# Performance work log

Measured on AMD Instinct MI355X. Metric: run time of the kernel, lower is better.

## Reference

```python
import jax, jax.numpy as jnp
import numpy as np

# Dimensions (from init_kwargs)
B, Q, C = 2, 40000, 128      # batch, BEV queries (200x200), d_model
NH, NP = 8, 4                 # n_heads, n_points per head
H, W = 90, 160                # value feature-map spatial shape (len = H*W)
HD = C // NH                  # head dim


def setup_inputs() -> dict:
    key = jax.random.key(0)
    ks = jax.random.split(key, 8)
    s = 0.02
    return {
        "query": jax.random.normal(ks[0], (B, Q, C), jnp.float32),
        "value": jax.random.normal(ks[1], (B, H * W, C), jnp.float32),
        "ref_points": jax.random.uniform(ks[2], (B, Q, 2), jnp.float32),  # normalized [0,1] (x, y)
        "W_value": jax.random.normal(ks[3], (C, C), jnp.float32) * s,
        "b_value": jnp.zeros((C,), jnp.float32),
        "W_offset": jax.random.normal(ks[4], (C, NH * NP * 2), jnp.float32) * s,
        "b_offset": jnp.zeros((NH * NP * 2,), jnp.float32),
        "W_attn": jax.random.normal(ks[5], (C, NH * NP), jnp.float32) * s,
        "b_attn": jnp.zeros((NH * NP,), jnp.float32),
        "W_out": jax.random.normal(ks[6], (C, C), jnp.float32) * s,
        "b_out": jnp.zeros((C,), jnp.float32),
    }


def _bilinear_sample(value, loc):
    """value: [B, H*W, NH, HD]; loc: [B, Q, NH, NP, 2] normalized in [0,1].
    Bilinear grid-sample with zero padding outside (align_corners=False).
    Returns [B, Q, NH, NP, HD]."""
    x = loc[..., 0] * W - 0.5
    y = loc[..., 1] * H - 0.5
    x0 = jnp.floor(x)
    y0 = jnp.floor(y)
    wx = x - x0
    wy = y - y0
    x0i = x0.astype(jnp.int32)
    y0i = y0.astype(jnp.int32)
    v = jnp.transpose(value, (0, 2, 1, 3))  # [B, NH, HW, HD] for per-head gather

    def corner(xi, yi, w):
        valid = ((xi >= 0) & (xi < W) & (yi >= 0) & (yi < H)).astype(value.dtype)
        idx = jnp.clip(yi, 0, H - 1) * W + jnp.clip(xi, 0, W - 1)  # [B, Q, NH, NP]
        i = jnp.transpose(idx, (0, 2, 1, 3))                        # [B, NH, Q, NP]
        g = jax.vmap(jax.vmap(lambda vb, ib: vb[ib]))(v, i)         # [B, NH, Q, NP, HD]
        g = jnp.transpose(g, (0, 2, 1, 3, 4))                       # [B, Q, NH, NP, HD]
        return g * (w * valid)[..., None]

    return (corner(x0i, y0i, (1.0 - wx) * (1.0 - wy))
            + corner(x0i + 1, y0i, wx * (1.0 - wy))
            + corner(x0i, y0i + 1, (1.0 - wx) * wy)
            + corner(x0i + 1, y0i + 1, wx * wy))


def reference(query, value, ref_points, W_value, b_value, W_offset, b_offset,
              W_attn, b_attn, W_out, b_out):
    # value projection, split into heads
    v = (value @ W_value + b_value).reshape(B, H * W, NH, HD)
    # per-query learned sampling offsets (in pixels) and attention weights
    offsets = (query @ W_offset + b_offset).reshape(B, Q, NH, NP, 2)
    attn = jax.nn.softmax((query @ W_attn + b_attn).reshape(B, Q, NH, NP), axis=-1)
    # sampling locations, normalized
    norm = jnp.array([W, H], jnp.float32)
    loc = ref_points[:, :, None, None, :] + offsets / norm  # [B, Q, NH, NP, 2]
    sampled = _bilinear_sample(v, loc)                       # [B, Q, NH, NP, HD]
    agg = jnp.einsum('bqhpd,bqhp->bqhd', sampled, attn).reshape(B, Q, C)
    return agg @ W_out + b_out
```

## Files before the change

### kernel.cpp

```cpp
#include <hip/hip_runtime.h>
#include <hip/hip_bf16.h>

#define BB 2
#define QQ 40000
#define CC 128
#define NHH 8
#define NPP 4
#define HH 90
#define WW 160
#define HWW (HH*WW)
#define BQ (BB*QQ)
#define BHW (BB*HWW)

typedef __attribute__((ext_vector_type(8))) short short8;
typedef __attribute__((ext_vector_type(4))) float f32x4;

static __device__ inline short f2bf(float f) {
    __hip_bfloat16 h = __float2bfloat16(f);
    return __builtin_bit_cast(short, h);
}

__global__ __launch_bounds__(256) void prep_weights(
    const float* __restrict__ Wv, const float* __restrict__ Wo,
    const float* __restrict__ Wa, const float* __restrict__ Wout,
    const float* __restrict__ bo, const float* __restrict__ ba,
    short* __restrict__ wtv, short* __restrict__ wcat,
    short* __restrict__ woutt, float* __restrict__ bcat)
{
    const int t = blockIdx.x * 256 + threadIdx.x;
    const int stride = gridDim.x * 256;
    for (int i = t; i < 128 * 128; i += stride) {
        int n = i >> 7, k = i & 127;
        wtv[i] = f2bf(Wv[k * 128 + n]);
    }
    for (int i = t; i < 96 * 128; i += stride) {
        int n = i >> 7, k = i & 127;
        float w = (n < 64) ? Wo[k * 64 + n] : Wa[k * 32 + (n - 64)];
        wcat[i] = f2bf(w);
    }
    for (int i = t; i < 128 * 128; i += stride) {
        int n = i >> 7, k = i & 127;
        woutt[i] = f2bf(Wout[k * 128 + n]);
    }
    if (t < 96) bcat[t] = (t < 64) ? bo[t] : ba[t - 64];
}

template<int N, bool XF32, bool OUT_BF16>
__global__ __launch_bounds__(256, 2) void gemm_pipe(
    const void* __restrict__ Xv, const short* __restrict__ Wt,
    const float* __restrict__ bias, void* __restrict__ Yv, int ntiles)
{
    constexpr int CT = N / 32;
    __shared__ short sW[N * 128];
    __shared__ short sX[128 * 128];
    const int tid = threadIdx.x;

    for (int i = tid; i < N * 16; i += 256) {
        int nn = i >> 4, c8 = (i & 15) * 8;
        short8 wv = reinterpret_cast<const short8*>(Wt)[i];
        *(short8*)((char*)sW + ((nn * 256 + c8 * 2) ^ ((nn & 7) << 4))) = wv;
    }

    const int lane = tid & 63, wid = tid >> 6;
    const int wr = wid >> 1, wc = wid & 1;
    const int l15 = lane & 15, lg = lane >> 4;

    float bvc[CT];
    #pragma unroll
    for (int ct = 0; ct < CT; ++ct) bvc[ct] = bias[wc * (N / 2) + ct * 16 + l15];

    float4 xf[16];
    short8 xb[8];

    int tile = blockIdx.x;
    if (tile < ntiles) {
        if (XF32) {
            const float4* src = reinterpret_cast<const float4*>((const float*)Xv) + (long)tile * 4096;
            #pragma unroll
            for (int j = 0; j < 16; ++j) xf[j] = src[j * 256 + tid];
        } else {
            const short8* src = reinterpret_cast<const short8*>((const short*)Xv) + (long)tile * 2048;
            #pragma unroll
            for (int j = 0; j < 8; ++j) xb[j] = src[j * 256 + tid];
        }
    }

    for (; tile < ntiles; tile += gridDim.x) {
        __syncthreads();
        if (XF32) {
            #pragma unroll
            for (int j = 0; j < 16; ++j) {
                int flat = j * 256 + tid;
                int row = flat >> 5, c4 = flat & 31;
                int byo = (row * 256 + c4 * 8) ^ ((row & 7) << 4);
                short* p = (short*)((char*)sX + byo);
                p[0] = f2bf(xf[j].x); p[1] = f2bf(xf[j].y);
                p[2] = f2bf(xf[j].z); p[3] = f2bf(xf[j].w);
            }
        } else {
            #pragma unroll
            for (int j = 0; j < 8; ++j) {
                int flat = j * 256 + tid;
                int row = flat >> 4, c8 = flat & 15;
                int byo = (row * 256 + c8 * 16) ^ ((row & 7) << 4);
                *(short8*)((char*)sX + byo) = xb[j];
            }
        }
        int nt = tile + gridDim.x;
        if (nt < ntiles) {
            if (XF32) {
                const float4* src = reinterpret_cast<const float4*>((const float*)Xv) + (long)nt * 4096;
                #pragma unroll
                for (int j = 0; j < 16; ++j) xf[j] = src[j * 256 + tid];
            } else {
                const short8* src = reinterpret_cast<const short8*>((const short*)Xv) + (long)nt * 2048;
                #pragma unroll
                for (int j = 0; j < 8; ++j) xb[j] = src[j * 256 + tid];
            }
        }
        __syncthreads();

        f32x4 acc[4][CT] = {};
        #pragma unroll
        for (int ks = 0; ks < 4; ++ks) {
            short8 a[4], b[CT];
            #pragma unroll
            for (int rt = 0; rt < 4; ++rt) {
                int row = wr * 64 + rt * 16 + l15;
                a[rt] = *(const short8*)((const char*)sX +
                        ((row * 256 + ks * 64 + lg * 16) ^ ((row & 7) << 4)));
            }
            #pragma unroll
            for (int ct = 0; ct < CT; ++ct) {
                int n = wc * (N / 2) + ct * 16 + l15;
                b[ct] = *(const short8*)((const char*)sW +
                        ((n * 256 + ks * 64 + lg * 16) ^ ((n & 7) << 4)));
            }
            #pragma unroll
            for (int rt = 0; rt < 4; ++rt)
                #pragma unroll
                for (int ct = 0; ct < CT; ++ct)
                    acc[rt][ct] = __builtin_amdgcn_mfma_f32_16x16x32_bf16(
                        a[rt], b[ct], acc[rt][ct], 0, 0, 0);
        }

        const long r0 = (long)tile * 128;
        #pragma unroll
        for (int rt = 0; rt < 4; ++rt) {
            #pragma unroll
            for (int ct = 0; ct < CT; ++ct) {
                int col = wc * (N / 2) + ct * 16 + l15;
                #pragma unroll
                for (int r = 0; r < 4; ++r) {
                    long row = r0 + wr * 64 + rt * 16 + lg * 4 + r;
                    float val = acc[rt][ct][r] + bvc[ct];
                    if (OUT_BF16) ((short*)Yv)[row * N + col] = f2bf(val);
                    else          ((float*)Yv)[row * N + col] = val;
                }
            }
        }
    }
}

__global__ __launch_bounds__(256) void deform_sample(
    const short* __restrict__ v,
    const float* __restrict__ qp,
    const float* __restrict__ ref,
    unsigned* __restrict__ agg)
{
    const int bq   = blockIdx.x * 4 + (threadIdx.x >> 6);
    const int lane = threadIdx.x & 63;
    const int h  = lane >> 3;
    const int dp = lane & 7;
    const int bsel = (bq >= QQ) ? 1 : 0;

    const float rx = ref[(long)bq * 2 + 0] * (float)WW - 0.5f;
    const float ry = ref[(long)bq * 2 + 1] * (float)HH - 0.5f;

    const float* al = qp + (long)bq * 96 + 64 + h * 4;
    float l0 = al[0], l1 = al[1], l2 = al[2], l3 = al[3];
    float m = fmaxf(fmaxf(l0, l1), fmaxf(l2, l3));
    float e0 = __expf(l0 - m), e1 = __expf(l1 - m);
    float e2 = __expf(l2 - m), e3 = __expf(l3 - m);
    float inv = 1.0f / (e0 + e1 + e2 + e3);
    float aw[4] = { e0 * inv, e1 * inv, e2 * inv, e3 * inv };

    const float* ob = qp + (long)bq * 96 + h * 8;
    const short* vb = v + (long)bsel * HWW * 128 + h * 16 + dp * 2;

    float acc0 = 0.0f, acc1 = 0.0f;
    #pragma unroll
    for (int p = 0; p < NPP; ++p) {
        float x = rx + ob[p * 2 + 0];
        float y = ry + ob[p * 2 + 1];
        float x0f = floorf(x), y0f = floorf(y);
        float wx = x - x0f, wy = y - y0f;
        int ix0 = (int)x0f, iy0 = (int)y0f;
        float a = aw[p];
        #pragma unroll
        for (int cy = 0; cy < 2; ++cy) {
            int iy = iy0 + cy;
            float wyc = cy ? wy : (1.0f - wy);
            bool vy = ((unsigned)iy < (unsigned)HH);
            int iyc = min(max(iy, 0), HH - 1);
            #pragma unroll
            for (int cx = 0; cx < 2; ++cx) {
                int ix = ix0 + cx;
                float wxc = cx ? wx : (1.0f - wx);
                bool vx = ((unsigned)ix < (unsigned)WW);
                int ixc = min(max(ix, 0), WW - 1);
                float wgt = (vx && vy) ? (a * wxc * wyc) : 0.0f;
                unsigned u = *reinterpret_cast<const unsigned*>(
                    vb + ((long)iyc * WW + ixc) * 128);
                float g0 = __builtin_bit_cast(float, u << 16);
                float g1 = __builtin_bit_cast(float, u & 0xffff0000u);
                acc0 += wgt * g0;
                acc1 += wgt * g1;
            }
        }
    }
    unsigned pk = (unsigned)(unsigned short)f2bf(acc0)
                | ((unsigned)(unsigned short)f2bf(acc1) << 16);
    agg[(long)bq * 64 + lane] = pk;
}

extern "C" void kernel_launch(void* const* d_in, const int* in_sizes, int n_in,
                              void* d_out, int out_size, void* d_ws, size_t ws_size,
                              hipStream_t stream) {
    const float* query = (const float*)d_in[0];
    const float* value = (const float*)d_in[1];
    const float* ref   = (const float*)d_in[2];
    const float* Wv    = (const float*)d_in[3];
    const float* bv    = (const float*)d_in[4];
    const float* Wo    = (const float*)d_in[5];
    const float* bo    = (const float*)d_in[6];
    const float* Wa    = (const float*)d_in[7];
    const float* ba    = (const float*)d_in[8];
    const float* Wout  = (const float*)d_in[9];
    const float* bout  = (const float*)d_in[10];
    float* out = (float*)d_out;

    char* ws = (char*)d_ws;
    short* vbf   = (short*)ws;  ws += (long)BHW * 128 * 2;
    short* wtv   = (short*)ws;  ws += 128 * 128 * 2;
    short* wcat  = (short*)ws;  ws += 96 * 128 * 2;
    short* woutt = (short*)ws;  ws += 128 * 128 * 2;
    float* bcat  = (float*)ws;  ws += 128 * 4;
    float* qp    = (float*)ws;  ws += (long)BQ * 96 * 4;
    unsigned* aggb = (unsigned*)ws;

    const int ntV = BHW / 128;
    const int ntQ = BQ / 128;
    const int gV = ntV < 512 ? ntV : 512;
    const int gQ = ntQ < 512 ? ntQ : 512;

    prep_weights<<<64, 256, 0, stream>>>(Wv, Wo, Wa, Wout, bo, ba,
                                         wtv, wcat, woutt, bcat);
    gemm_pipe<128, true, true><<<gV, 256, 0, stream>>>(value, wtv, bv, vbf, ntV);
    gemm_pipe<96, true, false><<<gQ, 256, 0, stream>>>(query, wcat, bcat, qp, ntQ);
    deform_sample<<<BQ / 4, 256, 0, stream>>>(vbf, qp, ref, aggb);
    gemm_pipe<128, false, false><<<gQ, 256, 0, stream>>>(aggb, woutt, bout, out, ntQ);
}
```

Before: 170.5 us.

## Fuse deformable sampling with output projection and store query projections as bf16

The sampling kernel and the output projection GEMM become one kernel. Each block samples 128 queries into a swizzled shared-memory bf16 tile, then multiplies it by the shared-memory output weights with MFMA, so the aggregated tensor no longer makes a round trip through global memory. Each lane now gathers 8 bf16 channels per corner with one 16-byte load instead of 2 channels, and the offset and logit projection is written in bf16 rather than fp32. The costs are lower precision for the offsets and logits, 64KB of LDS per block that limits occupancy, and fewer threads in flight to hide gather latency.

After: 164.1 us. 3.8% less time.

```diff
diff --git a/kernel.cpp b/kernel.cpp
--- a/kernel.cpp
+++ b/kernel.cpp
@@ -13,11 +13,15 @@
 #define BHW (BB*HWW)
 
 typedef __attribute__((ext_vector_type(8))) short short8;
+typedef __attribute__((ext_vector_type(4))) unsigned short ushortx4;
 typedef __attribute__((ext_vector_type(4))) float f32x4;
 
 static __device__ inline short f2bf(float f) {
     __hip_bfloat16 h = __float2bfloat16(f);
     return __builtin_bit_cast(short, h);
+}
+static __device__ inline float bfu(unsigned short u) {
+    return __builtin_bit_cast(float, ((unsigned)u) << 16);
 }
 
 __global__ __launch_bounds__(256) void prep_weights(
@@ -162,66 +166,128 @@
     }
 }
 
-__global__ __launch_bounds__(256) void deform_sample(
+__global__ __launch_bounds__(256, 2) void sample_out(
     const short* __restrict__ v,
-    const float* __restrict__ qp,
+    const short* __restrict__ qp,
     const float* __restrict__ ref,
-    unsigned* __restrict__ agg)
+    const short* __restrict__ Wt,
+    const float* __restrict__ bias,
+    float* __restrict__ out)
 {
-    const int bq   = blockIdx.x * 4 + (threadIdx.x >> 6);
-    const int lane = threadIdx.x & 63;
-    const int h  = lane >> 3;
-    const int dp = lane & 7;
-    const int bsel = (bq >= QQ) ? 1 : 0;
-
-    const float rx = ref[(long)bq * 2 + 0] * (float)WW - 0.5f;
-    const float ry = ref[(long)bq * 2 + 1] * (float)HH - 0.5f;
-
-    const float* al = qp + (long)bq * 96 + 64 + h * 4;
-    float l0 = al[0], l1 = al[1], l2 = al[2], l3 = al[3];
-    float m = fmaxf(fmaxf(l0, l1), fmaxf(l2, l3));
-    float e0 = __expf(l0 - m), e1 = __expf(l1 - m);
-    float e2 = __expf(l2 - m), e3 = __expf(l3 - m);
-    float inv = 1.0f / (e0 + e1 + e2 + e3);
-    float aw[4] = { e0 * inv, e1 * inv, e2 * inv, e3 * inv };
-
-    const float* ob = qp + (long)bq * 96 + h * 8;
-    const short* vb = v + (long)bsel * HWW * 128 + h * 16 + dp * 2;
-
-    float acc0 = 0.0f, acc1 = 0.0f;
+    __shared__ short sAgg[128 * 128];
+    __shared__ short sW[128 * 128];
+    const int tid = threadIdx.x;
+    const int lane = tid & 63, wid = tid >> 6;
+    const long tile0 = (long)blockIdx.x * 128;
+
+    for (int i = tid; i < 128 * 16; i += 256) {
+        int nn = i >> 4, c8 = (i & 15) * 8;
+        short8 wv = reinterpret_cast<const short8*>(Wt)[i];
+        *(short8*)((char*)sW + ((nn * 256 + c8 * 2) ^ ((nn & 7) << 4))) = wv;
+    }
+
+    const int q4 = lane >> 4;
+    const int l  = lane & 15;
+    const int h  = l >> 1;
+
     #pragma unroll
-    for (int p = 0; p < NPP; ++p) {
-        float x = rx + ob[p * 2 + 0];
-        float y = ry + ob[p * 2 + 1];
-        float x0f = floorf(x), y0f = floorf(y);
-        float wx = x - x0f, wy = y - y0f;
-        int ix0 = (int)x0f, iy0 = (int)y0f;
-        float a = aw[p];
-        #pragma unroll
-        for (int cy = 0; cy < 2; ++cy) {
-            int iy = iy0 + cy;
-            float wyc = cy ? wy : (1.0f - wy);
-            bool vy = ((unsigned)iy < (unsigned)HH);
-            int iyc = min(max(iy, 0), HH - 1);
-            #pragma unroll
-            for (int cx = 0; cx < 2; ++cx) {
-                int ix = ix0 + cx;
-                float wxc = cx ? wx : (1.0f - wx);
-                bool vx = ((unsigned)ix < (unsigned)WW);
-                int ixc = min(max(ix, 0), WW - 1);
-                float wgt = (vx && vy) ? (a * wxc * wyc) : 0.0f;
-                unsigned u = *reinterpret_cast<const unsigned*>(
-                    vb + ((long)iyc * WW + ixc) * 128);
-                float g0 = __builtin_bit_cast(float, u << 16);
-                float g1 = __builtin_bit_cast(float, u & 0xffff0000u);
-                acc0 += wgt * g0;
-                acc1 += wgt * g1;
-            }
-        }
-    }
-    unsigned pk = (unsigned)(unsigned short)f2bf(acc0)
-                | ((unsigned)(unsigned short)f2bf(acc1) << 16);
-    agg[(long)bq * 64 + lane] = pk;
+    for (int pass = 0; pass < 8; ++pass) {
+        const int lq = wid * 32 + pass * 4 + q4;
+        const long bq = tile0 + lq;
+        const int bsel = (bq >= QQ) ? 1 : 0;
+
+        const float rx = ref[bq * 2 + 0] * (float)WW - 0.5f;
+        const float ry = ref[bq * 2 + 1] * (float)HH - 0.5f;
+
+        const short* qpb = qp + bq * 96;
+        ushortx4 lg4 = *reinterpret_cast<const ushortx4*>(qpb + 64 + h * 4);
+        float l0 = bfu(lg4[0]), l1 = bfu(lg4[1]), l2 = bfu(lg4[2]), l3 = bfu(lg4[3]);
+        float m = fmaxf(fmaxf(l0, l1), fmaxf(l2, l3));
+        float e0 = __expf(l0 - m), e1 = __expf(l1 - m);
+        float e2 = __expf(l2 - m), e3 = __expf(l3 - m);
+        float inv = 1.0f / (e0 + e1 + e2 + e3);
+        float aw[4] = { e0 * inv, e1 * inv, e2 * inv, e3 * inv };
+
+        short8 ob = *reinterpret_cast<const short8*>(qpb + h * 8);
+        float ofs[8];
+        #pragma unroll
+        for (int j = 0; j < 8; ++j) ofs[j] = bfu((unsigned short)ob[j]);
+
+        const short* vb = v + (long)bsel * HWW * 128 + l * 8;
+
+        float ac[8] = {0,0,0,0,0,0,0,0};
+        #pragma unroll
+        for (int p = 0; p < NPP; ++p) {
+            float x = rx + ofs[p * 2 + 0];
+            float y = ry + ofs[p * 2 + 1];
+            float x0f = floorf(x), y0f = floorf(y);
+            float wx = x - x0f, wy = y - y0f;
+            int ix0 = (int)x0f, iy0 = (int)y0f;
+            float wxs[2] = { 1.0f - wx, wx };
+            float wys[2] = { 1.0f - wy, wy };
+            #pragma unroll
+            for (int cy = 0; cy < 2; ++cy) {
+                int iy = iy0 + cy;
+                bool vy = ((unsigned)iy < (unsigned)HH);
+                int iyc = min(max(iy, 0), HH - 1);
+                #pragma unroll
+                for (int cx = 0; cx < 2; ++cx) {
+                    int ix = ix0 + cx;
+                    bool vx = ((unsigned)ix < (unsigned)WW);
+                    int ixc = min(max(ix, 0), WW - 1);
+                    float wgt = (vx && vy) ? (aw[p] * wxs[cx] * wys[cy]) : 0.0f;
+                    short8 g = *reinterpret_cast<const short8*>(vb + (iyc * WW + ixc) * 128);
+                    #pragma unroll
+                    for (int j = 0; j < 8; ++j)
+                        ac[j] += wgt * bfu((unsigned short)g[j]);
+                }
+            }
+        }
+        short8 pk;
+        #pragma unroll
+        for (int j = 0; j < 8; ++j) pk[j] = f2bf(ac[j]);
+        *(short8*)((char*)sAgg + ((lq * 256 + l * 16) ^ ((lq & 7) << 4))) = pk;
+    }
+    __syncthreads();
+
+    const int wr = wid >> 1, wc = wid & 1;
+    const int l15 = lane & 15, lg = lane >> 4;
+    f32x4 acc[4][4] = {};
+    #pragma unroll
+    for (int ks = 0; ks < 4; ++ks) {
+        short8 a[4], b[4];
+        #pragma unroll
+        for (int rt = 0; rt < 4; ++rt) {
+            int row = wr * 64 + rt * 16 + l15;
+            a[rt] = *(const short8*)((const char*)sAgg +
+                    ((row * 256 + ks * 64 + lg * 16) ^ ((row & 7) << 4)));
+        }
+        #pragma unroll
+        for (int ct = 0; ct < 4; ++ct) {
+            int n = wc * 64 + ct * 16 + l15;
+            b[ct] = *(const short8*)((const char*)sW +
+                    ((n * 256 + ks * 64 + lg * 16) ^ ((n & 7) << 4)));
+        }
+        #pragma unroll
+        for (int rt = 0; rt < 4; ++rt)
+            #pragma unroll
+            for (int ct = 0; ct < 4; ++ct)
+                acc[rt][ct] = __builtin_amdgcn_mfma_f32_16x16x32_bf16(
+                    a[rt], b[ct], acc[rt][ct], 0, 0, 0);
+    }
+    #pragma unroll
+    for (int rt = 0; rt < 4; ++rt) {
+        #pragma unroll
+        for (int ct = 0; ct < 4; ++ct) {
+            int col = wc * 64 + ct * 16 + l15;
+            float bv = bias[col];
+            #pragma unroll
+            for (int r = 0; r < 4; ++r) {
+                long row = tile0 + wr * 64 + rt * 16 + lg * 4 + r;
+                out[row * 128 + col] = acc[rt][ct][r] + bv;
+            }
+        }
+    }
 }
 
 extern "C" void kernel_launch(void* const* d_in, const int* in_sizes, int n_in,
@@ -246,8 +312,7 @@
     short* wcat  = (short*)ws;  ws += 96 * 128 * 2;
     short* woutt = (short*)ws;  ws += 128 * 128 * 2;
     float* bcat  = (float*)ws;  ws += 128 * 4;
-    float* qp    = (float*)ws;  ws += (long)BQ * 96 * 4;
-    unsigned* aggb = (unsigned*)ws;
+    short* qpb   = (short*)ws;
 
     const int ntV = BHW / 128;
     const int ntQ = BQ / 128;
@@ -257,7 +322,6 @@
     prep_weights<<<64, 256, 0, stream>>>(Wv, Wo, Wa, Wout, bo, ba,
                                          wtv, wcat, woutt, bcat);
     gemm_pipe<128, true, true><<<gV, 256, 0, stream>>>(value, wtv, bv, vbf, ntV);
-    gemm_pipe<96, true, false><<<gQ, 256, 0, stream>>>(query, wcat, bcat, qp, ntQ);
-    deform_sample<<<BQ / 4, 256, 0, stream>>>(vbf, qp, ref, aggb);
-    gemm_pipe<128, false, false><<<gQ, 256, 0, stream>>>(aggb, woutt, bout, out, ntQ);
-}
+    gemm_pipe<96, true, true><<<gQ, 256, 0, stream>>>(query, wcat, bcat, qpb, ntQ);
+    sample_out<<<ntQ, 256, 0, stream>>>(vbf, qpb, ref, woutt, bout, out);
+}
```

## Store query projections in bf16 and sample 8 channels per thread

Applied to the files above, without the earlier changes.

The offset/attention projection now writes bf16 instead of fp32, which halves that intermediate buffer and its reads. The sampling kernel is remapped from one 64-lane wavefront per query with 2 channels per lane to 16 threads per query with 8 channels per lane, using 16-byte vector loads of value corners and a 16-byte store of the aggregate. Each thread now does more gathers and arithmetic, and more queries share a wavefront. Offsets in bf16 lose precision (pixel offsets rounded to about 8 mantissa bits), which may shift sampling locations slightly.

After: 161.6 us. -5.2%, faster.

```diff
diff --git a/kernel.cpp b/kernel.cpp
--- a/kernel.cpp
+++ b/kernel.cpp
@@ -13,11 +13,15 @@
 #define BHW (BB*HWW)
 
 typedef __attribute__((ext_vector_type(8))) short short8;
+typedef __attribute__((ext_vector_type(4))) unsigned short ushortx4;
 typedef __attribute__((ext_vector_type(4))) float f32x4;
 
 static __device__ inline short f2bf(float f) {
     __hip_bfloat16 h = __float2bfloat16(f);
     return __builtin_bit_cast(short, h);
+}
+static __device__ inline float bfu(unsigned short u) {
+    return __builtin_bit_cast(float, ((unsigned)u) << 16);
 }
 
 __global__ __launch_bounds__(256) void prep_weights(
@@ -162,66 +166,69 @@
     }
 }
 
-__global__ __launch_bounds__(256) void deform_sample(
+__global__ __launch_bounds__(256) void deform_sample16(
     const short* __restrict__ v,
-    const float* __restrict__ qp,
+    const short* __restrict__ qp,
     const float* __restrict__ ref,
-    unsigned* __restrict__ agg)
+    short* __restrict__ agg)
 {
-    const int bq   = blockIdx.x * 4 + (threadIdx.x >> 6);
-    const int lane = threadIdx.x & 63;
-    const int h  = lane >> 3;
-    const int dp = lane & 7;
-    const int bsel = (bq >= QQ) ? 1 : 0;
-
-    const float rx = ref[(long)bq * 2 + 0] * (float)WW - 0.5f;
-    const float ry = ref[(long)bq * 2 + 1] * (float)HH - 0.5f;
-
-    const float* al = qp + (long)bq * 96 + 64 + h * 4;
-    float l0 = al[0], l1 = al[1], l2 = al[2], l3 = al[3];
+    const int t = blockIdx.x * 256 + threadIdx.x;
+    const long q = t >> 4;
+    const int l = t & 15;
+    const int h = l >> 1;
+    const int bsel = (q >= QQ) ? 1 : 0;
+
+    const float rx = ref[q * 2 + 0] * (float)WW - 0.5f;
+    const float ry = ref[q * 2 + 1] * (float)HH - 0.5f;
+
+    const short* qpb = qp + q * 96;
+    ushortx4 lg4 = *reinterpret_cast<const ushortx4*>(qpb + 64 + h * 4);
+    float l0 = bfu(lg4[0]), l1 = bfu(lg4[1]), l2 = bfu(lg4[2]), l3 = bfu(lg4[3]);
     float m = fmaxf(fmaxf(l0, l1), fmaxf(l2, l3));
     float e0 = __expf(l0 - m), e1 = __expf(l1 - m);
     float e2 = __expf(l2 - m), e3 = __expf(l3 - m);
     float inv = 1.0f / (e0 + e1 + e2 + e3);
     float aw[4] = { e0 * inv, e1 * inv, e2 * inv, e3 * inv };
 
-    const float* ob = qp + (long)bq * 96 + h * 8;
-    const short* vb = v + (long)bsel * HWW * 128 + h * 16 + dp * 2;
-
-    float acc0 = 0.0f, acc1 = 0.0f;
+    short8 ob = *reinterpret_cast<const short8*>(qpb + h * 8);
+    float ofs[8];
+    #pragma unroll
+    for (int j = 0; j < 8; ++j) ofs[j] = bfu((unsigned short)ob[j]);
+
+    const short* vb = v + (long)bsel * HWW * 128 + l * 8;
+
+    float ac[8] = {0,0,0,0,0,0,0,0};
     #pragma unroll
     for (int p = 0; p < NPP; ++p) {
-        float x = rx + ob[p * 2 + 0];
-        float y = ry + ob[p * 2 + 1];
+        float x = rx + ofs[p * 2 + 0];
+        float y = ry + ofs[p * 2 + 1];
         float x0f = floorf(x), y0f = floorf(y);
         float wx = x - x0f, wy = y - y0f;
         int ix0 = (int)x0f, iy0 = (int)y0f;
-        float a = aw[p];
+        float wxs[2] = { 1.0f - wx, wx };
+        float wys[2] = { 1.0f - wy, wy };
         #pragma unroll
         for (int cy = 0; cy < 2; ++cy) {
             int iy = iy0 + cy;
-            float wyc = cy ? wy : (1.0f - wy);
             bool vy = ((unsigned)iy < (unsigned)HH);
             int iyc = min(max(iy, 0), HH - 1);
             #pragma unroll
             for (int cx = 0; cx < 2; ++cx) {
                 int ix = ix0 + cx;
-                float wxc = cx ? wx : (1.0f - wx);
                 bool vx = ((unsigned)ix < (unsigned)WW);
                 int ixc = min(max(ix, 0), WW - 1);
-                float wgt = (vx && vy) ? (a * wxc * wyc) : 0.0f;
-                unsigned u = *reinterpret_cast<const unsigned*>(
-                    vb + ((long)iyc * WW + ixc) * 128);
-                float g0 = __builtin_bit_cast(float, u << 16);
-                float g1 = __builtin_bit_cast(float, u & 0xffff0000u);
-                acc0 += wgt * g0;
-                acc1 += wgt * g1;
-            }
-        }
-    }
-    unsigned pk = (unsigned)(unsigned short)f2bf(acc0)
-                | ((unsigned)(unsigned short)f2bf(acc1) << 16);
-    agg[(long)bq * 64 + lane] = pk;
+                float wgt = (vx && vy) ? (aw[p] * wxs[cx] * wys[cy]) : 0.0f;
+                short8 g = *reinterpret_cast<const short8*>(vb + (iyc * WW + ixc) * 128);
+                #pragma unroll
+                for (int j = 0; j < 8; ++j)
+                    ac[j] += wgt * bfu((unsigned short)g[j]);
+            }
+        }
+    }
+    short8 pk;
+    #pragma unroll
+    for (int j = 0; j < 8; ++j) pk[j] = f2bf(ac[j]);
+    *reinterpret_cast<short8*>(agg + q * 128 + l * 8) = pk;
 }
 
 extern "C" void kernel_launch(void* const* d_in, const int* in_sizes, int n_in,
@@ -246,8 +253,8 @@
     short* wcat  = (short*)ws;  ws += 96 * 128 * 2;
     short* woutt = (short*)ws;  ws += 128 * 128 * 2;
     float* bcat  = (float*)ws;  ws += 128 * 4;
-    float* qp    = (float*)ws;  ws += (long)BQ * 96 * 4;
-    unsigned* aggb = (unsigned*)ws;
+    short* qpb   = (short*)ws;  ws += (long)BQ * 96 * 2;
+    short* aggb  = (short*)ws;
 
     const int ntV = BHW / 128;
     const int ntQ = BQ / 128;
@@ -257,7 +264,7 @@
     prep_weights<<<64, 256, 0, stream>>>(Wv, Wo, Wa, Wout, bo, ba,
                                          wtv, wcat, woutt, bcat);
     gemm_pipe<128, true, true><<<gV, 256, 0, stream>>>(value, wtv, bv, vbf, ntV);
-    gemm_pipe<96, true, false><<<gQ, 256, 0, stream>>>(query, wcat, bcat, qp, ntQ);
-    deform_sample<<<BQ / 4, 256, 0, stream>>>(vbf, qp, ref, aggb);
+    gemm_pipe<96, true, true><<<gQ, 256, 0, stream>>>(query, wcat, bcat, qpb, ntQ);
+    deform_sample16<<<(BQ * 16) / 256, 256, 0, stream>>>(vbf, qpb, ref, aggb);
     gemm_pipe<128, false, false><<<gQ, 256, 0, stream>>>(aggb, woutt, bout, out, ntQ);
 }
```
